# Optimization experiments

Hardware: AMD Instinct MI355X
Metric: run time of the kernel (lower is better)

The kernel has to match this reference:

```python
import jax, jax.numpy as jnp
import numpy as np

B, T, C, H = 4, 4096, 1024, 128

def setup_inputs() -> dict:
    key = jax.random.key(0)
    k1, k2, k3, k4 = jax.random.split(key, 4)
    s = 1.0 / np.sqrt(C)  # roughly match nn.Linear init scale
    return {
        "xd": jax.random.normal(k1, (B, T, C), dtype=jnp.float32),
        "Wq": jax.random.normal(k2, (C, H), dtype=jnp.float32) * s,
        "Wk": jax.random.normal(k3, (C, H), dtype=jnp.float32) * s,
        "Wv": jax.random.normal(k4, (C, H), dtype=jnp.float32) * s,
    }

def reference(xd, Wq, Wk, Wv):
    # self-attention path (xe is None): k, q, v all from xd
    q = jnp.einsum("btc,ch->bth", xd, Wq)
    k = jnp.einsum("btc,ch->bth", xd, Wk)
    v = jnp.einsum("btc,ch->bth", xd, Wv)
    scale = jnp.asarray(k.shape[-1], q.dtype) ** -0.5
    wei = jnp.einsum("bqh,bkh->bqk", q, k) * scale  # [B, T, T]
    # causal mask (masking=True): tril == 0 -> -inf
    causal = jnp.tril(jnp.ones((xd.shape[1], xd.shape[1]), dtype=bool))
    wei = jnp.where(causal[None, :, :], wei, jnp.asarray(-jnp.inf, wei.dtype))
    wei = jax.nn.softmax(wei, axis=-1)
    # dropout: eval-mode identity (deterministic reference)
    out = jnp.einsum("bqk,bkh->bqh", wei, v)  # [B, T, H]
    return out
```

## Files before the change

kernel.cpp:

```cpp
#include <hip/hip_runtime.h>
#include <math.h>

typedef __bf16 bf16x8 __attribute__((ext_vector_type(8)));
typedef float f32x4 __attribute__((ext_vector_type(4)));
typedef float f32x16 __attribute__((ext_vector_type(16)));
typedef unsigned int u32x4 __attribute__((ext_vector_type(4)));
typedef unsigned short u16x8 __attribute__((ext_vector_type(8)));

#define B_ 4
#define T_ 4096
#define C_ 1024
#define H_ 128

static __device__ __forceinline__ unsigned short f32_to_bf16(float f) {
  unsigned int u = __builtin_bit_cast(unsigned int, f);
  u += 0x7FFFu + ((u >> 16) & 1u);
  return (unsigned short)(u >> 16);
}
static __device__ __forceinline__ float bf16_to_f32(unsigned short u) {
  unsigned int x = ((unsigned int)u) << 16;
  return __builtin_bit_cast(float, x);
}

static __device__ __forceinline__ bf16x8 ld16g(const unsigned short* p) {
  return __builtin_bit_cast(bf16x8, *(const u32x4*)p);
}

static __device__ __forceinline__ f32x4 mfma16(bf16x8 a, bf16x8 b, f32x4 c) {
  return __builtin_amdgcn_mfma_f32_16x16x32_bf16(a, b, c, 0, 0, 0);
}
static __device__ __forceinline__ f32x16 mfma32(bf16x8 a, bf16x8 b, f32x16 c) {
  return __builtin_amdgcn_mfma_f32_32x32x16_bf16(a, b, c, 0, 0, 0);
}

static __device__ __forceinline__ void swapu(unsigned int& a, unsigned int& b) {
  asm volatile("v_permlane32_swap_b32 %0, %1" : "+v"(a), "+v"(b));
}
static __device__ __forceinline__ unsigned int cvtpk(float lo, float hi) {
  unsigned int r;
  asm("v_cvt_pk_bf16_f32 %0, %1, %2" : "=v"(r) : "v"(lo), "v"(hi));
  return r;
}
static __device__ __forceinline__ unsigned short cvt1(float v) {
  return (unsigned short)cvtpk(v, v);
}
static __device__ __forceinline__ float bpermf(int addr, float v) {
  return __builtin_bit_cast(float, __builtin_amdgcn_ds_bpermute(addr, __builtin_bit_cast(int, v)));
}
static __device__ __forceinline__ float half_merge_max(float x) {
  return fmaxf(x, __shfl_xor(x, 32));
}
static __device__ __forceinline__ float half_merge_sum(float x) {
  return x + __shfl_xor(x, 32);
}
static __device__ __forceinline__ float vmax16(f32x16 v) {
  float a0 = fmaxf(v[0], v[1]),  a1 = fmaxf(v[2], v[3]);
  float a2 = fmaxf(v[4], v[5]),  a3 = fmaxf(v[6], v[7]);
  float a4 = fmaxf(v[8], v[9]),  a5 = fmaxf(v[10], v[11]);
  float a6 = fmaxf(v[12], v[13]), a7 = fmaxf(v[14], v[15]);
  float b0 = fmaxf(a0, a1), b1 = fmaxf(a2, a3), b2 = fmaxf(a4, a5), b3 = fmaxf(a6, a7);
  return fmaxf(fmaxf(b0, b1), fmaxf(b2, b3));
}
static __device__ __forceinline__ float vsum16(f32x16 v) {
  float a0 = v[0] + v[1],  a1 = v[2] + v[3],  a2 = v[4] + v[5],  a3 = v[6] + v[7];
  float a4 = v[8] + v[9],  a5 = v[10] + v[11], a6 = v[12] + v[13], a7 = v[14] + v[15];
  float b0 = a0 + a1, b1 = a2 + a3, b2 = a4 + a5, b3 = a6 + a7;
  return (b0 + b1) + (b2 + b3);
}

typedef __attribute__((address_space(1))) const unsigned char as1_u8;
typedef __attribute__((address_space(3))) unsigned char as3_u8;
static __device__ __forceinline__ void async16(const void* g, void* l) {
  __builtin_amdgcn_global_load_lds((as1_u8*)g, (as3_u8*)l, 16, 0, 0);
}

static __device__ __forceinline__ u16x8 pack8cvt(float4 a, float4 b) {
  u32x4 u;
  u[0] = cvtpk(a.x, a.y); u[1] = cvtpk(a.z, a.w);
  u[2] = cvtpk(b.x, b.y); u[3] = cvtpk(b.z, b.w);
  return __builtin_bit_cast(u16x8, u);
}

#define PART_BYTES 33792

__global__ __launch_bounds__(256) void conv_w_kernel(const float* __restrict__ W0,
                                                     const float* __restrict__ W1,
                                                     const float* __restrict__ W2,
                                                     unsigned short* __restrict__ WT,
                                                     float qscale) {
  int tid = blockIdx.x * 256 + threadIdx.x;
  int o = tid >> 17;
  int r = tid & 131071;
  int n = r & 127;
  int k = r >> 7;
  const float* W = (o == 0) ? W0 : ((o == 1) ? W1 : W2);
  float v = W[r];
  if (o == 0) v *= qscale;
  WT[(size_t)o * 131072 + (size_t)n * 1024 + k] = f32_to_bf16(v);
}

__global__ __launch_bounds__(256) void qkv_fused_kernel(const float* __restrict__ X,
                                                        const unsigned short* __restrict__ WT,
                                                        unsigned short* __restrict__ Qb,
                                                        unsigned short* __restrict__ K3,
                                                        unsigned short* __restrict__ V3) {
  __shared__ __align__(16) unsigned short At[128 * 64];
  __shared__ __align__(16) unsigned short Bt[128 * 64];
  const int bid = blockIdx.x;
  const int xcd = bid & 7, ii = bid >> 3;
  const int o = ii % 3;
  const int tile = (ii / 3) * 8 + xcd;

  const float* Ax = X + (size_t)tile * 128 * 1024;
  const unsigned short* Bsrc = WT + (size_t)o * 131072;

  const int tid = threadIdx.x;
  const int lane = tid & 63, wid = tid >> 6;
  const int l15 = lane & 15, lg = lane >> 4;
  const int srow = wid * 8 + (lane >> 3);
  const int scol = (lane & 7) * 8;
  const int swcol = scol ^ ((srow & 7) << 3);
  const int sbcol = (((lane & 7) ^ (lane >> 3)) << 3);
  const int wm = wid >> 1, wn = wid & 1;
  const int rsw = (l15 & 7) << 3;

  const f32x4 fzero = {0.f, 0.f, 0.f, 0.f};
  f32x4 acc[4][4];
#pragma unroll
  for (int i = 0; i < 4; i++)
#pragma unroll
    for (int j = 0; j < 4; j++) acc[i][j] = fzero;

  float4 fA[4][2];
#pragma unroll
  for (int i4 = 0; i4 < 4; i4++) {
    const float* xs = Ax + (size_t)(i4 * 32 + srow) * 1024 + scol;
    fA[i4][0] = *(const float4*)xs;
    fA[i4][1] = *(const float4*)(xs + 4);
  }

  for (int ks = 0; ks < 16; ks++) {
    const int k0 = ks * 64;
    __syncthreads();
#pragma unroll
    for (int i4 = 0; i4 < 4; i4++)
      async16(Bsrc + (size_t)(i4 * 32 + srow) * 1024 + k0 + sbcol, &Bt[(i4 * 32 + wid * 8) * 64]);
#pragma unroll
    for (int i4 = 0; i4 < 4; i4++) {
      const int row = i4 * 32 + srow;
      *(u16x8*)(&At[row * 64 + swcol]) = pack8cvt(fA[i4][0], fA[i4][1]);
    }
    __syncthreads();
    if (ks + 1 < 16) {
#pragma unroll
      for (int i4 = 0; i4 < 4; i4++) {
        const float* xs = Ax + (size_t)(i4 * 32 + srow) * 1024 + (ks + 1) * 64 + scol;
        fA[i4][0] = *(const float4*)xs;
        fA[i4][1] = *(const float4*)(xs + 4);
      }
    }
#pragma unroll
    for (int kk = 0; kk < 2; kk++) {
      bf16x8 af[4], bfr[4];
#pragma unroll
      for (int i = 0; i < 4; i++)
        af[i] = ld16g(&At[(wm * 64 + i * 16 + l15) * 64 + ((kk * 32 + lg * 8) ^ rsw)]);
#pragma unroll
      for (int j = 0; j < 4; j++)
        bfr[j] = ld16g(&Bt[(wn * 64 + j * 16 + l15) * 64 + ((kk * 32 + lg * 8) ^ rsw)]);
      __builtin_amdgcn_s_setprio(1);
#pragma unroll
      for (int i = 0; i < 4; i++)
#pragma unroll
        for (int j = 0; j < 4; j++) acc[i][j] = mfma16(af[i], bfr[j], acc[i][j]);
      __builtin_amdgcn_s_setprio(0);
    }
  }

  if (o == 0) {
#pragma unroll
    for (int i = 0; i < 4; i++)
#pragma unroll
      for (int j = 0; j < 4; j++)
#pragma unroll
        for (int r = 0; r < 4; r++) {
          int row = tile * 128 + wm * 64 + i * 16 + lg * 4 + r;
          int col = wn * 64 + j * 16 + l15;
          Qb[(size_t)row * 128 + col] = cvt1(acc[i][j][r]);
        }
  } else if (o == 1) {
#pragma unroll
    for (int i = 0; i < 4; i++)
#pragma unroll
      for (int j = 0; j < 4; j++)
#pragma unroll
        for (int r = 0; r < 4; r++) {
          int token = tile * 128 + wm * 64 + i * 16 + lg * 4 + r;
          int d = wn * 64 + j * 16 + l15;
          int bb = token >> 12, t = token & 4095;
          int t32 = t >> 5;
          int lane2 = (t & 31) | (((d >> 3) & 1) << 5);
          int c = d >> 4;
          int j2 = d & 7;
          K3[(size_t)(((bb * 128 + t32) * 8 + c) * 64 + lane2) * 8 + j2] = cvt1(acc[i][j][r]);
        }
  } else {
#pragma unroll
    for (int i = 0; i < 4; i++)
#pragma unroll
      for (int j = 0; j < 4; j++)
#pragma unroll
        for (int r = 0; r < 4; r++) {
          int token = tile * 128 + wm * 64 + i * 16 + lg * 4 + r;
          int d = wn * 64 + j * 16 + l15;
          int bb = token >> 12, tt = token & 4095;
          int t32 = tt >> 5;
          int kss = (tt >> 4) & 1;
          int hi2 = (tt >> 3) & 1;
          int j2 = tt & 7;
          int dt = d >> 5;
          int lane2 = (d & 31) | (hi2 << 5);
          V3[(size_t)(((bb * 128 + t32) * 8 + dt * 2 + kss) * 64 + lane2) * 8 + j2] = cvt1(acc[i][j][r]);
        }
  }
}

__global__ __launch_bounds__(256, 2) void attn_kernel(const unsigned short* __restrict__ Qb,
                                                      const unsigned short* __restrict__ K3,
                                                      const unsigned short* __restrict__ V3,
                                                      unsigned char* __restrict__ Pw8) {
  const int bid = blockIdx.x;
  const int xcd = bid & 7;
  const int b = xcd >> 1;
  const int rest = bid >> 3;
  const int h = rest % 6;
  const int jj = rest / 6;
  const int g = (xcd & 1) + 2 * (15 - jj);

  const int tid = threadIdx.x;
  const int wid = tid >> 6, lane = tid & 63;
  const int l31 = lane & 31, hi = lane >> 5;
  const int qbase = g * 128 + wid * 32;

  __shared__ __align__(16) unsigned char LDSraw[32768];
  unsigned short* lbuf = (unsigned short*)LDSraw;

  const unsigned short* K3b = K3 + (size_t)b * 524288;
  const unsigned short* V3b = V3 + (size_t)b * 524288;
  const int jmax_w = 4 * g + wid;
  const int Jcap = 4 * g + 3;
  const int R = (Jcap >= h) ? ((Jcap - h) / 6 + 1) : 0;

  const unsigned short* qp = Qb + ((size_t)(b * T_ + qbase + l31) << 7) + hi * 8;
  bf16x8 qf[8];
#pragma unroll
  for (int c = 0; c < 8; c++) qf[c] = ld16g(qp + c * 16);

  const f32x16 z16 = {0.f,0.f,0.f,0.f,0.f,0.f,0.f,0.f,0.f,0.f,0.f,0.f,0.f,0.f,0.f,0.f};
  f32x16 o[4];
  o[0] = z16; o[1] = z16; o[2] = z16; o[3] = z16;
  float m = -1e30f, l = 0.f;
  const int addrbase = hi << 4;

  const unsigned short* sbase = (wid < 2) ? K3b : V3b;
  const int soff = (wid & 1) * 2048;
  const int region = ((wid >= 2) ? 4096 : 0) + soff;

  if (R > 0) {
    const unsigned short* s0 = sbase + (size_t)h * 4096 + soff + lane * 8;
    unsigned short* d0 = lbuf + region;
#pragma unroll
    for (int i = 0; i < 4; i++) async16(s0 + i * 512, d0 + i * 512);
  }

  for (int r = 0; r < R; r++) {
    const int cur = r & 1;
    if (r + 1 < R) {
      const int jS = h + 6 * (r + 1);
      const unsigned short* sN = sbase + (size_t)jS * 4096 + soff + lane * 8;
      unsigned short* dN = lbuf + (cur ^ 1) * 8192 + region;
#pragma unroll
      for (int i = 0; i < 4; i++) async16(sN + i * 512, dN + i * 512);
      asm volatile("s_waitcnt vmcnt(4)" ::: "memory");
    } else {
      asm volatile("s_waitcnt vmcnt(0)" ::: "memory");
    }
    __builtin_amdgcn_s_barrier();

    const int j = h + 6 * r;
    if (j <= jmax_w) {
      const unsigned short* Kl = lbuf + cur * 8192;
      const unsigned short* Vl = Kl + 4096;
      bf16x8 kf[8];
#pragma unroll
      for (int c = 0; c < 8; c++) kf[c] = ld16g(Kl + c * 512 + lane * 8);
      f32x16 s = z16;
      __builtin_amdgcn_s_setprio(1);
#pragma unroll
      for (int c = 0; c < 8; c++) s = mfma32(kf[c], qf[c], s);
      __builtin_amdgcn_s_setprio(0);

      bf16x8 vf[4][2];
#pragma unroll
      for (int dt = 0; dt < 4; dt++)
#pragma unroll
        for (int ks = 0; ks < 2; ks++)
          vf[dt][ks] = ld16g(Vl + (dt * 2 + ks) * 512 + lane * 8);

      if (j == jmax_w) {
        const int kvb = j << 5;
        const int qq = qbase + l31;
#pragma unroll
        for (int r2 = 0; r2 < 16; r2++) {
          const int c0 = (r2 & 3) + 8 * (r2 >> 2) + 4 * hi;
          if (kvb + c0 > qq) s[r2] = -1e30f;
        }
      }

      float pm = half_merge_max(vmax16(s));
      const bool skip = __all(pm - m <= 8.0f);
      float mn = skip ? m : fmaxf(m, pm);
#pragma unroll
      for (int r2 = 0; r2 < 16; r2++) s[r2] = exp2f(s[r2] - mn);
      float ps = half_merge_sum(vsum16(s));
      if (skip) {
        l = l + ps;
      } else {
        float al = exp2f(m - mn);
        m = mn;
        l = l * al + ps;
#pragma unroll
        for (int r2 = 0; r2 < 16; r2++) {
          const int addr = addrbase + 4 * ((r2 & 3) + 8 * (r2 >> 2));
          float alb = bpermf(addr, al);
          o[0][r2] *= alb; o[1][r2] *= alb; o[2][r2] *= alb; o[3][r2] *= alb;
        }
      }

      bf16x8 pa[2];
#pragma unroll
      for (int ks = 0; ks < 2; ks++) {
        const int gb = ks * 8;
        unsigned int xa = cvtpk(s[gb + 0], s[gb + 1]), xb = cvtpk(s[gb + 4], s[gb + 5]);
        swapu(xa, xb);
        unsigned int ya = cvtpk(s[gb + 2], s[gb + 3]), yb = cvtpk(s[gb + 6], s[gb + 7]);
        swapu(ya, yb);
        u32x4 pw; pw[0] = xa; pw[1] = ya; pw[2] = xb; pw[3] = yb;
        pa[ks] = __builtin_bit_cast(bf16x8, pw);
      }

      __builtin_amdgcn_s_setprio(1);
#pragma unroll
      for (int ks = 0; ks < 2; ks++)
#pragma unroll
        for (int dt = 0; dt < 4; dt++) o[dt] = mfma32(pa[ks], vf[dt][ks], o[dt]);
      __builtin_amdgcn_s_setprio(0);
    }
    __builtin_amdgcn_sched_barrier(0);
    __builtin_amdgcn_s_barrier();
  }

  unsigned char* Pb = Pw8 + (size_t)((b * 32 + g) * 6 + h) * PART_BYTES;
  unsigned short* Po = (unsigned short*)Pb;
  float* Pm = (float*)(Pb + 32768);
  float* Pl = (float*)(Pb + 33280);
#pragma unroll
  for (int r2 = 0; r2 < 16; r2++) {
    const int q128 = wid * 32 + (r2 & 3) + 8 * (r2 >> 2) + 4 * hi;
#pragma unroll
    for (int dt = 0; dt < 4; dt++)
      Po[q128 * 128 + dt * 32 + l31] = cvt1(o[dt][r2]);
  }
  if (lane < 32) { Pm[wid * 32 + l31] = m; Pl[wid * 32 + l31] = l; }
}

__global__ __launch_bounds__(256) void attn_merge_kernel(const unsigned char* __restrict__ Pw8,
                                                         float* __restrict__ Out) {
  const int bid = blockIdx.x;
  const int xcd = bid & 7, idx = bid >> 3;
  const int b = xcd >> 1;
  const int g = ((idx >> 4) << 1) | (xcd & 1);
  const int tl = b * 32 + g;
  const int inner = (idx & 15) * 256 + threadIdx.x;
  const int q = inner >> 5;
  const int d = (inner & 31) * 4;
  const unsigned char* base = Pw8 + (size_t)tl * 6 * PART_BYTES;

  float mm[6], ll[6];
#pragma unroll
  for (int p = 0; p < 6; p++) {
    mm[p] = *(const float*)(base + p * PART_BYTES + 32768 + q * 4);
    ll[p] = *(const float*)(base + p * PART_BYTES + 33280 + q * 4);
  }
  float mn = mm[0];
#pragma unroll
  for (int p = 1; p < 6; p++) mn = fmaxf(mn, mm[p]);
  float f[6], denom = 0.f;
#pragma unroll
  for (int p = 0; p < 6; p++) { f[p] = exp2f(mm[p] - mn); denom += f[p] * ll[p]; }
  const float inv = 1.0f / denom;

  f32x4 acc = {0.f, 0.f, 0.f, 0.f};
#pragma unroll
  for (int p = 0; p < 6; p++) {
    const unsigned short* po = (const unsigned short*)(base + p * PART_BYTES) + q * 128 + d;
    unsigned long long v4 = *(const unsigned long long*)po;
    const unsigned short* pv = (const unsigned short*)&v4;
#pragma unroll
    for (int i = 0; i < 4; i++) acc[i] += f[p] * bf16_to_f32(pv[i]);
  }
#pragma unroll
  for (int i = 0; i < 4; i++) acc[i] *= inv;
  *(f32x4*)(Out + (size_t)(b * 4096 + g * 128 + q) * 128 + d) = acc;
}

extern "C" void kernel_launch(void* const* d_in, const int* in_sizes, int n_in,
                              void* d_out, int out_size, void* d_ws, size_t ws_size,
                              hipStream_t stream) {
  const float* X  = (const float*)d_in[0];
  const float* W0 = (const float*)d_in[1];
  const float* W1 = (const float*)d_in[2];
  const float* W2 = (const float*)d_in[3];
  float* Out = (float*)d_out;

  unsigned char* ws = (unsigned char*)d_ws;
  unsigned short* WT = (unsigned short*)(ws);
  unsigned char* Pw  = ws;
  unsigned short* Qb = (unsigned short*)(ws + 34078720);
  unsigned short* K3 = (unsigned short*)(ws + 38273024);
  unsigned short* V3 = (unsigned short*)(ws + 42467328);

  const float qscale = 1.4426950408889634f / sqrtf(128.0f);

  conv_w_kernel<<<dim3(1536), dim3(256), 0, stream>>>(W0, W1, W2, WT, qscale);
  qkv_fused_kernel<<<dim3(384), dim3(256), 0, stream>>>(X, WT, Qb, K3, V3);
  attn_kernel<<<dim3(768), dim3(256), 0, stream>>>(Qb, K3, V3, Pw);
  attn_merge_kernel<<<dim3(2048), dim3(256), 0, stream>>>(Pw, Out);
}
```

Measured before the change: 72.01 us.

## Load QKV GEMM operands directly into registers, dropping LDS staging and barriers

The QKV projection kernel no longer stages A and B tiles through shared memory with two barriers per k-step. Each wave now loads its own MFMA fragments straight from global memory into registers, converting X to bf16 in registers, with double-buffered register banks for B and a prefetch of the next k-step. This removes LDS traffic and block synchronisation. In exchange, waves sharing rows or columns re-read the same data from global/L2 (about 2x redundant loads), uses more registers, and the per-lane global accesses are 16-32 byte strided chunks rather than fully coalesced rows.

```diff
diff --git a/kernel.cpp b/kernel.cpp
--- a/kernel.cpp
+++ b/kernel.cpp
@@ -74,11 +74,11 @@
   __builtin_amdgcn_global_load_lds((as1_u8*)g, (as3_u8*)l, 16, 0, 0);
 }
 
-static __device__ __forceinline__ u16x8 pack8cvt(float4 a, float4 b) {
+static __device__ __forceinline__ bf16x8 cvt8(float4 a, float4 b) {
   u32x4 u;
   u[0] = cvtpk(a.x, a.y); u[1] = cvtpk(a.z, a.w);
   u[2] = cvtpk(b.x, b.y); u[3] = cvtpk(b.z, b.w);
-  return __builtin_bit_cast(u16x8, u);
+  return __builtin_bit_cast(bf16x8, u);
 }
 
 #define PART_BYTES 33792
@@ -99,13 +99,51 @@
   WT[(size_t)o * 131072 + (size_t)n * 1024 + k] = f32_to_bf16(v);
 }
 
+#define QKV_LOAD_A(KS)                                                        \
+  _Pragma("unroll")                                                           \
+  for (int i = 0; i < 4; i++)                                                 \
+    _Pragma("unroll")                                                         \
+    for (int kk = 0; kk < 2; kk++) {                                          \
+      const float* ap = a_base + (size_t)i * 16384 + (KS) * 64 + kk * 32;     \
+      fA[i][kk][0] = *(const float4*)ap;                                      \
+      fA[i][kk][1] = *(const float4*)(ap + 4);                                \
+    }
+
+#define QKV_LOAD_B(BANK, KS)                                                  \
+  _Pragma("unroll")                                                           \
+  for (int j = 0; j < 4; j++)                                                 \
+    _Pragma("unroll")                                                         \
+    for (int kk = 0; kk < 2; kk++)                                            \
+      BANK[j][kk] = ld16g(b_base + (size_t)j * 16384 + (KS) * 64 + kk * 32);
+
+#define QKV_STEP(KS, BCUR, BNXT)                                              \
+  {                                                                           \
+    bf16x8 af[4][2];                                                          \
+    _Pragma("unroll")                                                         \
+    for (int i = 0; i < 4; i++)                                               \
+      _Pragma("unroll")                                                       \
+      for (int kk = 0; kk < 2; kk++)                                          \
+        af[i][kk] = cvt8(fA[i][kk][0], fA[i][kk][1]);                         \
+    if ((KS) + 1 < 16) {                                                      \
+      QKV_LOAD_A((KS) + 1)                                                    \
+      QKV_LOAD_B(BNXT, (KS) + 1)                                              \
+    }                                                                         \
+    __builtin_amdgcn_s_setprio(1);                                            \
+    _Pragma("unroll")                                                         \
+    for (int kk = 0; kk < 2; kk++)                                            \
+      _Pragma("unroll")                                                       \
+      for (int i = 0; i < 4; i++)                                             \
+        _Pragma("unroll")                                                     \
+        for (int j = 0; j < 4; j++)                                           \
+          acc[i][j] = mfma16(af[i][kk], BCUR[j][kk], acc[i][j]);              \
+    __builtin_amdgcn_s_setprio(0);                                            \
+  }
+
 __global__ __launch_bounds__(256) void qkv_fused_kernel(const float* __restrict__ X,
                                                         const unsigned short* __restrict__ WT,
                                                         unsigned short* __restrict__ Qb,
                                                         unsigned short* __restrict__ K3,
                                                         unsigned short* __restrict__ V3) {
-  __shared__ __align__(16) unsigned short At[128 * 64];
-  __shared__ __align__(16) unsigned short Bt[128 * 64];
   const int bid = blockIdx.x;
   const int xcd = bid & 7, ii = bid >> 3;
   const int o = ii % 3;
@@ -117,12 +155,10 @@
   const int tid = threadIdx.x;
   const int lane = tid & 63, wid = tid >> 6;
   const int l15 = lane & 15, lg = lane >> 4;
-  const int srow = wid * 8 + (lane >> 3);
-  const int scol = (lane & 7) * 8;
-  const int swcol = scol ^ ((srow & 7) << 3);
-  const int sbcol = (((lane & 7) ^ (lane >> 3)) << 3);
   const int wm = wid >> 1, wn = wid & 1;
-  const int rsw = (l15 & 7) << 3;
+
+  const float* a_base = Ax + (size_t)(wm * 64 + l15) * 1024 + lg * 8;
+  const unsigned short* b_base = Bsrc + (size_t)(wn * 64 + l15) * 1024 + lg * 8;
 
   const f32x4 fzero = {0.f, 0.f, 0.f, 0.f};
   f32x4 acc[4][4];
@@ -131,50 +167,15 @@
 #pragma unroll
     for (int j = 0; j < 4; j++) acc[i][j] = fzero;
 
-  float4 fA[4][2];
-#pragma unroll
-  for (int i4 = 0; i4 < 4; i4++) {
-    const float* xs = Ax + (size_t)(i4 * 32 + srow) * 1024 + scol;
-    fA[i4][0] = *(const float4*)xs;
-    fA[i4][1] = *(const float4*)(xs + 4);
-  }
-
-  for (int ks = 0; ks < 16; ks++) {
-    const int k0 = ks * 64;
-    __syncthreads();
-#pragma unroll
-    for (int i4 = 0; i4 < 4; i4++)
-      async16(Bsrc + (size_t)(i4 * 32 + srow) * 1024 + k0 + sbcol, &Bt[(i4 * 32 + wid * 8) * 64]);
-#pragma unroll
-    for (int i4 = 0; i4 < 4; i4++) {
-      const int row = i4 * 32 + srow;
-      *(u16x8*)(&At[row * 64 + swcol]) = pack8cvt(fA[i4][0], fA[i4][1]);
-    }
-    __syncthreads();
-    if (ks + 1 < 16) {
-#pragma unroll
-      for (int i4 = 0; i4 < 4; i4++) {
-        const float* xs = Ax + (size_t)(i4 * 32 + srow) * 1024 + (ks + 1) * 64 + scol;
-        fA[i4][0] = *(const float4*)xs;
-        fA[i4][1] = *(const float4*)(xs + 4);
-      }
-    }
-#pragma unroll
-    for (int kk = 0; kk < 2; kk++) {
-      bf16x8 af[4], bfr[4];
-#pragma unroll
-      for (int i = 0; i < 4; i++)
-        af[i] = ld16g(&At[(wm * 64 + i * 16 + l15) * 64 + ((kk * 32 + lg * 8) ^ rsw)]);
-#pragma unroll
-      for (int j = 0; j < 4; j++)
-        bfr[j] = ld16g(&Bt[(wn * 64 + j * 16 + l15) * 64 + ((kk * 32 + lg * 8) ^ rsw)]);
-      __builtin_amdgcn_s_setprio(1);
-#pragma unroll
-      for (int i = 0; i < 4; i++)
-#pragma unroll
-        for (int j = 0; j < 4; j++) acc[i][j] = mfma16(af[i], bfr[j], acc[i][j]);
-      __builtin_amdgcn_s_setprio(0);
-    }
+  float4 fA[4][2][2];
+  bf16x8 bA[4][2], bB[4][2];
+
+  QKV_LOAD_A(0)
+  QKV_LOAD_B(bA, 0)
+
+  for (int ks = 0; ks < 16; ks += 2) {
+    QKV_STEP(ks,     bA, bB)
+    QKV_STEP(ks + 1, bB, bA)
   }
 
   if (o == 0) {
```

Result: slower. 134.4 us (+86.6%).
